# Kernel optimization log

Hardware: AMD Instinct MI355X
Metric: run time of the kernel (lower is better)

The kernel has to match this reference:

```python
import jax, jax.numpy as jnp
import numpy as np

# FP8 E4M3 constants (per FP8Handler)
E4M3_MAX = 240.0          # max_normal
MANTISSA_SCALE = 8.0      # 2 ** mantissa_bits (3)
SCALE_EPS = 1e-10


def setup_inputs() -> dict:
    key = jax.random.key(0)
    k1, k2, k3 = jax.random.split(key, 3)
    B, S, D_IN, D_OUT = 4, 2048, 4096, 4096
    x = jax.random.normal(k1, (B, S, D_IN), dtype=jnp.float32)
    weight = jax.random.normal(k2, (D_OUT, D_IN), dtype=jnp.float32)
    bias = jax.random.normal(k3, (D_OUT,), dtype=jnp.float32)
    return {"x": x, "weight": weight, "bias": bias}


def _fp8_e4m3_quant_dequant(w, scale):
    # FP8Handler.quantize_tensor + _simulate_e4m3_precision
    s = jnp.clip(w / scale, -E4M3_MAX, E4M3_MAX)
    s = s.astype(jnp.float16).astype(jnp.float32)  # fp16 round-trip
    q = jnp.round(s * MANTISSA_SCALE) / MANTISSA_SCALE  # mantissa truncation
    q = jnp.clip(q, -E4M3_MAX, E4M3_MAX)
    return q * scale


def reference(x, weight, bias):
    # FP8Quantizer.compute_scale: per-tensor max-abs, margin=0, fresh history
    amax = jnp.max(jnp.abs(weight))
    scale = jnp.maximum(amax / E4M3_MAX, SCALE_EPS)
    qw = _fp8_e4m3_quant_dequant(weight, scale)  # [out, in]
    # F.linear(x, qw, bias): x [b, s, in] @ qw.T [in, out] + bias
    return jnp.einsum('bsi,oi->bso', x, qw) + bias
```

## Files before the change

### kernel.cpp

```cpp
#include <hip/hip_runtime.h>
#include <hip/hip_bf16.h>
#include <hip/hip_fp16.h>

#define E4M3_MAX 240.0f

typedef __attribute__((ext_vector_type(8))) __bf16 bf16x8;
typedef __attribute__((ext_vector_type(16))) float f32x16;
typedef unsigned short ushort_t;

__device__ __forceinline__ void gload_lds16(const void* g, void* l) {
  __builtin_amdgcn_global_load_lds(
      (const __attribute__((address_space(1))) void*)g,
      (__attribute__((address_space(3))) void*)l,
      16, 0, 0);
}

__global__ void amax_abs_kernel(const float* __restrict__ w, int n4,
                                unsigned* __restrict__ amax_bits) {
  float m = 0.0f;
  const float4* w4 = (const float4*)w;
  int stride = gridDim.x * blockDim.x;
  for (int i = blockIdx.x * blockDim.x + threadIdx.x; i < n4; i += stride) {
    float4 v = w4[i];
    m = fmaxf(m, fmaxf(fmaxf(fabsf(v.x), fabsf(v.y)),
                       fmaxf(fabsf(v.z), fabsf(v.w))));
  }
  for (int off = 32; off > 0; off >>= 1)
    m = fmaxf(m, __shfl_down(m, off, 64));
  __shared__ float smax[4];
  int l = threadIdx.x & 63, wv = threadIdx.x >> 6;
  if (l == 0) smax[wv] = m;
  __syncthreads();
  if (threadIdx.x == 0) {
    float bm = fmaxf(fmaxf(smax[0], smax[1]), fmaxf(smax[2], smax[3]));
    atomicMax(amax_bits, __float_as_uint(bm));
  }
}

__global__ void quant_weight_kernel(const float* __restrict__ w,
                                    const unsigned* __restrict__ amax_bits,
                                    ushort_t* __restrict__ qw, int n4) {
  float amax = __uint_as_float(*amax_bits);
  float scale = fmaxf(amax / E4M3_MAX, 1e-10f);
  const float4* w4 = (const float4*)w;
  ushort4* q4 = (ushort4*)qw;
  int stride = gridDim.x * blockDim.x;
  for (int i = blockIdx.x * blockDim.x + threadIdx.x; i < n4; i += stride) {
    float4 v = w4[i];
    float r[4] = {v.x, v.y, v.z, v.w};
    ushort_t o[4];
#pragma unroll
    for (int j = 0; j < 4; ++j) {
      float s = fminf(fmaxf(r[j] / scale, -E4M3_MAX), E4M3_MAX);
      s = __half2float(__float2half(s));
      float q = rintf(s * 8.0f) * 0.125f;
      q = fminf(fmaxf(q, -E4M3_MAX), E4M3_MAX);
      __hip_bfloat16 h = __float2bfloat16(q * scale);
      o[j] = *(ushort_t*)&h;
    }
    ushort4 ov = {o[0], o[1], o[2], o[3]};
    q4[i] = ov;
  }
}

__global__ void cvt_bf16_kernel(const float* __restrict__ x,
                                ushort_t* __restrict__ xb, int n4) {
  const float4* x4 = (const float4*)x;
  ushort4* o4 = (ushort4*)xb;
  int stride = gridDim.x * blockDim.x;
  for (int i = blockIdx.x * blockDim.x + threadIdx.x; i < n4; i += stride) {
    float4 v = x4[i];
    __hip_bfloat16 h0 = __float2bfloat16(v.x);
    __hip_bfloat16 h1 = __float2bfloat16(v.y);
    __hip_bfloat16 h2 = __float2bfloat16(v.z);
    __hip_bfloat16 h3 = __float2bfloat16(v.w);
    ushort4 o = {*(ushort_t*)&h0, *(ushort_t*)&h1,
                 *(ushort_t*)&h2, *(ushort_t*)&h3};
    o4[i] = o;
  }
}


#define BAR() do { asm volatile("" ::: "memory"); \
                   __builtin_amdgcn_s_barrier(); \
                   asm volatile("" ::: "memory"); } while (0)
#define LGKM0() asm volatile("s_waitcnt lgkmcnt(0)" ::: "memory")
#define LGKM8() asm volatile("s_waitcnt lgkmcnt(8)" ::: "memory")
#define VMC4() asm volatile("s_waitcnt vmcnt(4)" ::: "memory")
#define VMC0() asm volatile("s_waitcnt vmcnt(0)" ::: "memory")
#define NOVM() do {} while (0)

__global__ __launch_bounds__(512, 2) void gemm256_w32(
    const ushort_t* __restrict__ A, const ushort_t* __restrict__ Bt,
    const float* __restrict__ bias, float* __restrict__ C) {
  constexpr int K = 4096, N = 4096;
  __shared__ __align__(16) ushort_t As[2][2][8192];
  __shared__ __align__(16) ushort_t Bs[2][2][8192];

  const int tid = threadIdx.x;
  const int wid = tid >> 6, lane = tid & 63;
  const int wm = wid >> 2, wn = wid & 3;
  const int l31 = lane & 31, lk2 = lane >> 5;

  int bid = blockIdx.x;
  int swz = (bid & 7) * 64 + (bid >> 3);
  int bm = swz >> 4, bn = swz & 15;

  const ushort_t* Ab = A + (size_t)bm * 256 * K;
  const ushort_t* Bb = Bt + (size_t)bn * 256 * K;

  int offG[2];
#pragma unroll
  for (int q = 0; q < 2; ++q) {
    int s = q * 512 + tid;
    int row = s >> 3;
    int c = (s & 7) ^ (row & 7) ^ ((row >> 3) & 3);
    offG[q] = row * K + c * 8;
  }

#define STAGE_AH(buf, kt, h)                                               \
  do { _Pragma("unroll") for (int q = 0; q < 2; ++q)                       \
    gload_lds16(Ab + (size_t)(h) * 128 * K + (kt) * 64 + offG[q],          \
                &As[buf][h][(q * 512 + wid * 64) * 8]); } while (0)
#define STAGE_BH(buf, kt, h)                                               \
  do { _Pragma("unroll") for (int q = 0; q < 2; ++q)                       \
    gload_lds16(Bb + (size_t)(h) * 128 * K + (kt) * 64 + offG[q],          \
                &Bs[buf][h][(q * 512 + wid * 64) * 8]); } while (0)

  const int bhalf = wn >> 1;
  const int brow0 = (wn & 1) * 64;
  const int sig = (l31 & 7) ^ ((l31 >> 3) & 3);
  int xks[4];
#pragma unroll
  for (int ks = 0; ks < 4; ++ks) xks[ks] = ((ks * 2 + lk2) ^ sig) * 8;

  bf16x8 af[4][4], bf[2][4];
  f32x16 acc[4][2] = {};

#define RD_A32(buf, rg)                                                    \
  do { _Pragma("unroll") for (int ks = 0; ks < 4; ++ks)                    \
    af[rg][ks] = *(const bf16x8*)                                          \
        &As[buf][wm][((rg) * 32 + l31) * 64 + xks[ks]]; } while (0)
#define RD_B32(buf)                                                        \
  do { _Pragma("unroll") for (int cg = 0; cg < 2; ++cg)                    \
    _Pragma("unroll") for (int ks = 0; ks < 4; ++ks)                       \
      bf[cg][ks] = *(const bf16x8*)                                        \
          &Bs[buf][bhalf][(brow0 + cg * 32 + l31) * 64 + xks[ks]]; } while (0)

#define MMA8(rg)                                                           \
  do { __builtin_amdgcn_s_setprio(1);                                      \
    _Pragma("unroll") for (int ks = 0; ks < 4; ++ks) {                     \
      acc[rg][0] = __builtin_amdgcn_mfma_f32_32x32x16_bf16(                \
          af[rg][ks], bf[0][ks], acc[rg][0], 0, 0, 0);                     \
      acc[rg][1] = __builtin_amdgcn_mfma_f32_32x32x16_bf16(                \
          af[rg][ks], bf[1][ks], acc[rg][1], 0, 0, 0);                     \
    }                                                                      \
    __builtin_amdgcn_s_setprio(0); } while (0)

#define ITER(t, SB1, SA2, SB2, SA3, VM4, VM8)                              \
  do {                                                                     \
    RD_B32(0); RD_A32(0, 0);                                               \
    if (SB1) STAGE_BH(1, (t) + 1, 0);                                      \
    LGKM8(); BAR(); LGKM0(); MMA8(0); BAR();                               \
    RD_A32(0, 1); RD_A32(0, 2); RD_A32(0, 3);                              \
    if (SB1) STAGE_BH(1, (t) + 1, 1);                                      \
    LGKM8(); BAR(); LGKM0(); MMA8(1); BAR();                               \
    if (SA2) STAGE_AH(0, (t) + 2, 0);                                      \
    BAR(); MMA8(2); BAR();                                                 \
    if (SA2) STAGE_AH(0, (t) + 2, 1);                                      \
    BAR(); MMA8(3); VM4; BAR();                                            \
    RD_B32(1); RD_A32(1, 0);                                               \
    if (SB2) STAGE_BH(0, (t) + 2, 0);                                      \
    LGKM8(); BAR(); LGKM0(); MMA8(0); BAR();                               \
    RD_A32(1, 1); RD_A32(1, 2); RD_A32(1, 3);                              \
    if (SB2) STAGE_BH(0, (t) + 2, 1);                                      \
    LGKM8(); BAR(); LGKM0(); MMA8(1); BAR();                               \
    if (SA3) STAGE_AH(1, (t) + 3, 0);                                      \
    BAR(); MMA8(2); BAR();                                                 \
    if (SA3) STAGE_AH(1, (t) + 3, 1);                                      \
    BAR(); MMA8(3); VM8; BAR();                                            \
  } while (0)

  STAGE_AH(0, 0, 0); STAGE_AH(0, 0, 1);
  STAGE_BH(0, 0, 0); STAGE_BH(0, 0, 1);
  STAGE_AH(1, 1, 0); STAGE_AH(1, 1, 1);
  VMC4();
  BAR();

  for (int t = 0; t < 62; t += 2)
    ITER(t, 1, 1, 1, 1, VMC4(), VMC4());

  ITER(62, 1, 0, 0, 0, VMC0(), NOVM());

  float* Cb = C + (size_t)(bm * 256 + wm * 128) * N + bn * 256 + wn * 64;
#pragma unroll
  for (int cg = 0; cg < 2; ++cg) {
    int n = cg * 32 + l31;
    float bv = bias[bn * 256 + wn * 64 + n];
#pragma unroll
    for (int rg = 0; rg < 4; ++rg) {
#pragma unroll
      for (int r = 0; r < 16; ++r) {
        int row = rg * 32 + (r & 3) + 8 * (r >> 2) + 4 * lk2;
        Cb[(size_t)row * N + n] = acc[rg][cg][r] + bv;
      }
    }
  }
}

extern "C" void kernel_launch(void* const* d_in, const int* in_sizes, int n_in,
                              void* d_out, int out_size, void* d_ws, size_t ws_size,
                              hipStream_t stream) {
  const float* x = (const float*)d_in[0];
  const float* wt = (const float*)d_in[1];
  const float* bias = (const float*)d_in[2];
  float* out = (float*)d_out;

  const int DIN = 4096;
  const int NW = in_sizes[1];
  const int M = in_sizes[0] / DIN;

  char* ws = (char*)d_ws;
  unsigned* amax_bits = (unsigned*)ws;
  ushort_t* qw = (ushort_t*)(ws + 256);
  ushort_t* xb = (ushort_t*)(ws + 256 + (size_t)NW * 2);

  hipMemsetAsync(amax_bits, 0, 4, stream);
  hipLaunchKernelGGL(amax_abs_kernel, dim3(1024), dim3(256), 0, stream,
                     wt, NW / 4, amax_bits);
  hipLaunchKernelGGL(quant_weight_kernel, dim3(2048), dim3(256), 0, stream,
                     wt, amax_bits, qw, NW / 4);
  hipLaunchKernelGGL(cvt_bf16_kernel, dim3(2048), dim3(256), 0, stream,
                     x, xb, (M * DIN) / 4);

  hipLaunchKernelGGL(gemm256_w32, dim3(512), dim3(512), 0, stream,
                     xb, qw, bias, out);
}
```

Before: 328.2 us.

## Restructure GEMM main loop to one barrier per K-tile with double-buffered staging

Replaces the multi-barrier interleaved pipeline, which held two K-tiles of prefetch in flight and had barriers around every MFMA group, with a simpler schedule. Each K-tile now reads all fragments from LDS, issues the global-to-LDS loads for the next tile into the other buffer, runs the four MFMA groups gated by staged lgkmcnt waits, then waits for vmcnt(0) and takes a single barrier. The aim is to cut barrier and synchronisation overhead. In exchange, prefetch depth drops to one tile and every tile ends with a full vmcnt(0) wait, which can expose global-load latency.

```diff
diff --git a/kernel.cpp b/kernel.cpp
--- a/kernel.cpp
+++ b/kernel.cpp
@@ -84,13 +84,11 @@
 #define BAR() do { asm volatile("" ::: "memory"); \
                    __builtin_amdgcn_s_barrier(); \
                    asm volatile("" ::: "memory"); } while (0)
-#define LGKM0() asm volatile("s_waitcnt lgkmcnt(0)" ::: "memory")
-#define LGKM8() asm volatile("s_waitcnt lgkmcnt(8)" ::: "memory")
-#define VMC4() asm volatile("s_waitcnt vmcnt(4)" ::: "memory")
+#define FEN() asm volatile("" ::: "memory")
+#define LGKM(n) asm volatile("s_waitcnt lgkmcnt(" #n ")" ::: "memory")
 #define VMC0() asm volatile("s_waitcnt vmcnt(0)" ::: "memory")
-#define NOVM() do {} while (0)
-
-__global__ __launch_bounds__(512, 2) void gemm256_w32(
+
+__global__ __launch_bounds__(512, 2) void gemm256_1bar(
     const ushort_t* __restrict__ A, const ushort_t* __restrict__ Bt,
     const float* __restrict__ bias, float* __restrict__ C) {
   constexpr int K = 4096, N = 4096;
@@ -157,40 +155,34 @@
     }                                                                      \
     __builtin_amdgcn_s_setprio(0); } while (0)
 
-#define ITER(t, SB1, SA2, SB2, SA3, VM4, VM8)                              \
+#define TILE(cb, u, DO_S)                                                  \
   do {                                                                     \
-    RD_B32(0); RD_A32(0, 0);                                               \
-    if (SB1) STAGE_BH(1, (t) + 1, 0);                                      \
-    LGKM8(); BAR(); LGKM0(); MMA8(0); BAR();                               \
-    RD_A32(0, 1); RD_A32(0, 2); RD_A32(0, 3);                              \
-    if (SB1) STAGE_BH(1, (t) + 1, 1);                                      \
-    LGKM8(); BAR(); LGKM0(); MMA8(1); BAR();                               \
-    if (SA2) STAGE_AH(0, (t) + 2, 0);                                      \
-    BAR(); MMA8(2); BAR();                                                 \
-    if (SA2) STAGE_AH(0, (t) + 2, 1);                                      \
-    BAR(); MMA8(3); VM4; BAR();                                            \
-    RD_B32(1); RD_A32(1, 0);                                               \
-    if (SB2) STAGE_BH(0, (t) + 2, 0);                                      \
-    LGKM8(); BAR(); LGKM0(); MMA8(0); BAR();                               \
-    RD_A32(1, 1); RD_A32(1, 2); RD_A32(1, 3);                              \
-    if (SB2) STAGE_BH(0, (t) + 2, 1);                                      \
-    LGKM8(); BAR(); LGKM0(); MMA8(1); BAR();                               \
-    if (SA3) STAGE_AH(1, (t) + 3, 0);                                      \
-    BAR(); MMA8(2); BAR();                                                 \
-    if (SA3) STAGE_AH(1, (t) + 3, 1);                                      \
-    BAR(); MMA8(3); VM8; BAR();                                            \
+    RD_B32(cb); RD_A32(cb, 0); FEN();               \
+    RD_A32(cb, 1); FEN();                                  \
+    RD_A32(cb, 2); FEN();                                  \
+    RD_A32(cb, 3);                                         \
+    if (DO_S) {                                                            \
+      STAGE_AH((cb) ^ 1, (u) + 1, 0); STAGE_AH((cb) ^ 1, (u) + 1, 1);      \
+      STAGE_BH((cb) ^ 1, (u) + 1, 0); STAGE_BH((cb) ^ 1, (u) + 1, 1);      \
+    }                                                                      \
+    LGKM(12); MMA8(0);                                                     \
+    LGKM(8);  MMA8(1);                                                     \
+    LGKM(4);  MMA8(2);                                                     \
+    LGKM(0);  MMA8(3);                                                     \
+    VMC0(); BAR();                                                         \
   } while (0)
 
   STAGE_AH(0, 0, 0); STAGE_AH(0, 0, 1);
   STAGE_BH(0, 0, 0); STAGE_BH(0, 0, 1);
-  STAGE_AH(1, 1, 0); STAGE_AH(1, 1, 1);
-  VMC4();
+  VMC0();
   BAR();
 
-  for (int t = 0; t < 62; t += 2)
-    ITER(t, 1, 1, 1, 1, VMC4(), VMC4());
-
-  ITER(62, 1, 0, 0, 0, VMC0(), NOVM());
+  for (int t = 0; t < 62; t += 2) {
+    TILE(0, t, 1);
+    TILE(1, t + 1, 1);
+  }
+  TILE(0, 62, 1);
+  TILE(1, 63, 0);
 
   float* Cb = C + (size_t)(bm * 256 + wm * 128) * N + bn * 256 + wn * 64;
 #pragma unroll
@@ -233,6 +225,6 @@
   hipLaunchKernelGGL(cvt_bf16_kernel, dim3(2048), dim3(256), 0, stream,
                      x, xb, (M * DIN) / 4);
 
-  hipLaunchKernelGGL(gemm256_w32, dim3(512), dim3(512), 0, stream,
+  hipLaunchKernelGGL(gemm256_1bar, dim3(512), dim3(512), 0, stream,
                      xb, qw, bias, out);
 }
```

After: 365.9 us. 11.5% more time.
